# Kernel tuning notes

Measured on AMD Instinct MI355X. Metric: run time of the kernel, lower is better.

The kernel has to match this reference:

```python
import jax, jax.numpy as jnp
import numpy as np
from jax import lax

B, S, D, F = 2, 4096, 1024, 4096
LN_EPS = 1e-6

def _layer_norm(x, scale, bias):
    mu = jnp.mean(x, axis=-1, keepdims=True)
    var = jnp.mean(jnp.square(x - mu), axis=-1, keepdims=True)
    return (x - mu) * lax.rsqrt(var + LN_EPS) * scale + bias

def _gate_loop(q, k, v, a):
    # max-headed GateLoop: one head per channel, scalar complex state per channel
    # h_t = a_t * h_{t-1} + k_t * v_t ; y_t = q_t * h_t
    kv = (k * v).astype(jnp.complex64)
    def comb(e1, e2):
        a1, x1 = e1
        a2, x2 = e2
        return (a1 * a2, a2 * x1 + x2)
    _, h = lax.associative_scan(comb, (a, kv), axis=1)
    return q.astype(jnp.complex64) * h

def setup_inputs() -> dict:
    key = jax.random.key(0)
    ks = jax.random.split(key, 12)
    sd = 1.0 / np.sqrt(D)
    sf = 1.0 / np.sqrt(F)
    return {
        "x": jax.random.normal(ks[0], (B, S, D), jnp.float32),
        "Wq": jax.random.normal(ks[1], (D, D), jnp.float32) * sd,
        "Wk": jax.random.normal(ks[2], (D, D), jnp.float32) * sd,
        "Wv": jax.random.normal(ks[3], (D, D), jnp.float32) * sd,
        "Wa": jax.random.normal(ks[4], (D, 2 * D), jnp.float32) * sd,
        "Wg": jax.random.normal(ks[5], (D, D), jnp.float32) * sd,
        "Wo": jax.random.normal(ks[6], (D, D), jnp.float32) * sd,
        "ln1_scale": jnp.ones((D,), jnp.float32),
        "ln1_bias": jnp.zeros((D,), jnp.float32),
        "W1": jax.random.normal(ks[7], (D, F), jnp.float32) * sd,
        "b1": jax.random.normal(ks[8], (F,), jnp.float32) * 1e-6,
        "W2": jax.random.normal(ks[9], (F, D), jnp.float32) * sf,
        "b2": jax.random.normal(ks[10], (D,), jnp.float32) * 1e-6,
        "ln2_scale": jnp.ones((D,), jnp.float32),
        "ln2_bias": jnp.zeros((D,), jnp.float32),
    }

def reference(x, Wq, Wk, Wv, Wa, Wg, Wo, ln1_scale, ln1_bias, W1, b1, W2, b2, ln2_scale, ln2_bias):
    q = x @ Wq
    k = x @ Wk
    v = x @ Wv
    a = x @ Wa
    a_real, a_imag = jnp.split(a, 2, axis=-1)
    a_c = a_real + 1j * a_imag
    magnitude = jnp.abs(a_c)
    phase = jnp.angle(a_c)
    a_c = jax.nn.sigmoid(magnitude).astype(jnp.complex64) * jnp.exp(1j * phase)
    g = x.astype(jnp.complex64) @ Wg.astype(jnp.complex64)
    y = _gate_loop(q, k, v, a_c)
    y = y * (g * jax.nn.sigmoid(g))  # silu on complex g
    y = y @ Wo.astype(jnp.complex64)
    y = y.real
    # dropout deterministic (training=False)
    y = _layer_norm(y + x, ln1_scale, ln1_bias)
    h = jax.nn.gelu(y @ W1 + b1)
    out = h @ W2 + b2
    out = _layer_norm(out + y, ln2_scale, ln2_bias)
    return out
```

## Files before the change

### kernel.cpp

```cpp
#include <hip/hip_runtime.h>
#include <cstdint>

typedef unsigned short u16;
typedef unsigned int u32;

#define AS1 __attribute__((address_space(1)))
#define AS3 __attribute__((address_space(3)))

typedef _Float16 f16x8 __attribute__((ext_vector_type(8)));
typedef float f32x4 __attribute__((ext_vector_type(4)));

static constexpr int Bb = 2, Ss = 4096, Dd = 1024, Ff = 4096;
static constexpr int Mtok = Bb * Ss;
static constexpr int NCH = 128;
static constexpr int TCH = Ss / NCH;
static constexpr int PW = 6144;

__device__ __forceinline__ float h2f(u16 u) {
    union { u16 u; _Float16 h; } w; w.u = u; return (float)w.h;
}
__device__ __forceinline__ u16 f2h(float f) {
    union { _Float16 h; u16 u; } w; w.h = (_Float16)f; return w.u;
}

__device__ __forceinline__ float gelu_fast(float v) {
    float u = 1.5957691216057308f * (v + 0.044715f * v * v * v);
    return v / (1.f + __expf(-u));
}

__device__ __forceinline__ void gload_lds16(const u16* g, u16* l) {
    __builtin_amdgcn_global_load_lds((const AS1 u32*)g, (AS3 u32*)l, 16, 0, 0);
}

__global__ __launch_bounds__(256) void prep_fused(
    const float* __restrict__ x, u16* __restrict__ xb,
    const float* __restrict__ Wq, const float* __restrict__ Wk,
    const float* __restrict__ Wv, const float* __restrict__ Wa,
    const float* __restrict__ Wg, const float* __restrict__ Wo,
    const float* __restrict__ W1, const float* __restrict__ W2,
    u16* __restrict__ WTcat, u16* __restrict__ WTo,
    u16* __restrict__ WT1, u16* __restrict__ WT2) {
    __shared__ u16 t[32][33];
    const int tid = threadIdx.x;
    const int idx = blockIdx.x;
    if (idx < 8192) {
        const long i = ((long)idx * 256 + tid) * 4;
        float4 f = *(const float4*)(x + i);
        ushort4 o;
        o.x = f2h(f.x); o.y = f2h(f.y); o.z = f2h(f.z); o.w = f2h(f.w);
        *(ushort4*)(xb + i) = o;
        return;
    }
    const float* src; u16* dst; int K, N, ti;
    if (idx < 9216)       { src = Wq; dst = WTcat;             K = 1024; N = 1024; ti = idx - 8192; }
    else if (idx < 10240) { src = Wk; dst = WTcat + (1u << 20); K = 1024; N = 1024; ti = idx - 9216; }
    else if (idx < 11264) { src = Wv; dst = WTcat + (2u << 20); K = 1024; N = 1024; ti = idx - 10240; }
    else if (idx < 13312) { src = Wa; dst = WTcat + (3u << 20); K = 1024; N = 2048; ti = idx - 11264; }
    else if (idx < 14336) { src = Wg; dst = WTcat + (5u << 20); K = 1024; N = 1024; ti = idx - 13312; }
    else if (idx < 15360) { src = Wo; dst = WTo;               K = 1024; N = 1024; ti = idx - 14336; }
    else if (idx < 19456) { src = W1; dst = WT1;               K = 1024; N = 4096; ti = idx - 15360; }
    else                  { src = W2; dst = WT2;               K = 4096; N = 1024; ti = idx - 19456; }
    const int tiles_x = N >> 5;
    const int bx = ti % tiles_x, by = ti / tiles_x;
    const int n0 = bx << 5, k0 = by << 5;
    const int tx = tid & 31, ty = tid >> 5;
#pragma unroll
    for (int r = 0; r < 4; r++) {
        const int row = ty + r * 8;
        t[row][tx] = f2h(src[(long)(k0 + row) * N + n0 + tx]);
    }
    __syncthreads();
    const int cx = (tid & 15) << 1;
    const int ry = tid >> 4;
#pragma unroll
    for (int r = 0; r < 2; r++) {
        const int row = ry + r * 16;
        u32 v = (u32)t[cx][row] | ((u32)t[cx + 1][row] << 16);
        *(u32*)(dst + (long)(n0 + row) * K + k0 + cx) = v;
    }
}

template <int EPI>
__global__ __launch_bounds__(512, 2) void gemm8p(const u16* __restrict__ A,
                                                 const u16* __restrict__ BT,
                                                 u16* __restrict__ C,
                                                 const float* __restrict__ bias,
                                                 int M, int N, int K,
                                                 int lda, int ldc) {
    extern __shared__ u16 lds[];
    const int tid = threadIdx.x;

    const int ntn = N >> 8;
    const int total = (M >> 8) * ntn;
    const int tpb = total / (int)gridDim.x;
    const int cpx = total >> 3;

    const int srow = tid >> 3;
    const int scol = ((tid & 7) ^ (srow & 7)) << 3;
    const long lda64 = (long)lda << 6;
    const long ldb64 = (long)K << 6;

    const int nt = K >> 6;

    auto bases_for = [&](int t, int& tm, int& tn, const u16*& Ab, const u16*& Bb) {
        if (t > tpb - 1) t = tpb - 1;
        const int ti = (int)blockIdx.x + t * (int)gridDim.x;
        const int b = (ti & 7) * cpx + (ti >> 3);
        tm = (b / ntn) << 8;
        tn = (b % ntn) << 8;
        Ab = A + (long)(tm + srow) * lda + scol;
        Bb = BT + (long)(tn + srow) * (long)K + scol;
    };

    auto stA = [&](u16* bufbase, int h, const u16* Ab, int kt) {
        u16* d = bufbase + h * 8192 + tid * 8;
        const u16* g = Ab + (long)(h * 128) * lda + (kt << 6);
        gload_lds16(g, d);
        gload_lds16(g + lda64, d + 4096);
    };
    auto stB = [&](u16* bufbase, int h, const u16* Bb, int kt) {
        u16* d = bufbase + 16384 + h * 8192 + tid * 8;
        const u16* g = Bb + (long)(h * 128) * (long)K + (kt << 6);
        gload_lds16(g, d);
        gload_lds16(g + ldb64, d + 4096);
    };

    const int wid = tid >> 6, lane = tid & 63;
    const int r16 = lane & 15, q = lane >> 4;
    const int wm = (wid >> 2) * 128;
    const int wn = (wid & 3) * 64;
    const int r7 = r16 & 7;
    const int cx0 = (q ^ r7) << 3;
    const int cx1 = ((4 | q) ^ r7) << 3;
    const int aoff = (wm + r16) * 64;
    const int boff = 16384 + (wn + r16) * 64;

    f32x4 acc[8][4];
#pragma unroll
    for (int i = 0; i < 8; i++)
#pragma unroll
        for (int j = 0; j < 4; j++) acc[i][j] = (f32x4){0.f, 0.f, 0.f, 0.f};

    int tmc, tnc, tmn, tnn;
    const u16 *Ac, *Bc, *An, *Bn;
    bases_for(0, tmc, tnc, Ac, Bc);
    bases_for(1, tmn, tnn, An, Bn);

    stA(lds, 0, Ac, 0);
    stA(lds, 1, Ac, 0);
    stB(lds, 0, Bc, 0);
    stB(lds, 1, Bc, 0);
    stB(lds + 32768, 0, Bc, 1);
    stB(lds + 32768, 1, Bc, 1);

    for (int t = 0; t < tpb; ++t) {
        for (int it = 0; it < nt; ++it) {
            u16* sb = lds + ((it & 1) << 15);
            u16* so = lds + (((it & 1) ^ 1) << 15);

            asm volatile("s_waitcnt vmcnt(4)" ::: "memory");
            __builtin_amdgcn_s_barrier();

            f16x8 vb[4][2];
#pragma unroll
            for (int ni = 0; ni < 4; ni++) {
                vb[ni][0] = *(const f16x8*)(sb + boff + ni * 1024 + cx0);
                vb[ni][1] = *(const f16x8*)(sb + boff + ni * 1024 + cx1);
            }
            f16x8 pa[4][2];
#pragma unroll
            for (int m = 0; m < 4; m++) {
                pa[m][0] = *(const f16x8*)(sb + aoff + m * 1024 + cx0);
                pa[m][1] = *(const f16x8*)(sb + aoff + m * 1024 + cx1);
            }
            if (it + 1 < nt) {
                stA(so, 0, Ac, it + 1);
                stA(so, 1, Ac, it + 1);
            } else {
                stA(so, 0, An, 0);
                stA(so, 1, An, 0);
            }
            __builtin_amdgcn_s_barrier();
            asm volatile("s_waitcnt lgkmcnt(0)" ::: "memory");
            __builtin_amdgcn_s_setprio(1);
#pragma unroll
            for (int m = 0; m < 4; m++)
#pragma unroll
                for (int ni = 0; ni < 4; ni++) {
                    acc[m][ni] = __builtin_amdgcn_mfma_f32_16x16x32_f16(
                        pa[m][0], vb[ni][0], acc[m][ni], 0, 0, 0);
                    acc[m][ni] = __builtin_amdgcn_mfma_f32_16x16x32_f16(
                        pa[m][1], vb[ni][1], acc[m][ni], 0, 0, 0);
                }
            __builtin_amdgcn_s_setprio(0);
            __builtin_amdgcn_s_barrier();

#pragma unroll
            for (int m = 0; m < 4; m++) {
                pa[m][0] = *(const f16x8*)(sb + aoff + (4 + m) * 1024 + cx0);
                pa[m][1] = *(const f16x8*)(sb + aoff + (4 + m) * 1024 + cx1);
            }
            if (it + 2 < nt) {
                stB(sb, 0, Bc, it + 2);
                stB(sb, 1, Bc, it + 2);
            } else {
                stB(sb, 0, Bn, it + 2 - nt);
                stB(sb, 1, Bn, it + 2 - nt);
            }
            __builtin_amdgcn_s_barrier();
            asm volatile("s_waitcnt lgkmcnt(0)" ::: "memory");
            __builtin_amdgcn_s_setprio(1);
#pragma unroll
            for (int m = 0; m < 4; m++)
#pragma unroll
                for (int ni = 0; ni < 4; ni++) {
                    acc[4 + m][ni] = __builtin_amdgcn_mfma_f32_16x16x32_f16(
                        pa[m][0], vb[ni][0], acc[4 + m][ni], 0, 0, 0);
                    acc[4 + m][ni] = __builtin_amdgcn_mfma_f32_16x16x32_f16(
                        pa[m][1], vb[ni][1], acc[4 + m][ni], 0, 0, 0);
                }
            __builtin_amdgcn_s_setprio(0);
            __builtin_amdgcn_s_barrier();
        }

#pragma unroll
        for (int mi = 0; mi < 8; mi++) {
#pragma unroll
            for (int ni = 0; ni < 4; ni++) {
                const int gcol = tnc + wn + ni * 16 + r16;
                float bv = 0.f;
                if (EPI) bv = bias[gcol];
#pragma unroll
                for (int j = 0; j < 4; j++) {
                    const int grow = tmc + wm + mi * 16 + q * 4 + j;
                    float v = acc[mi][ni][j];
                    if (EPI) v += bv;
                    if (EPI == 1) v = gelu_fast(v);
                    C[(long)grow * ldc + gcol] = f2h(v);
                    acc[mi][ni][j] = 0.f;
                }
            }
        }
        tmc = tmn; tnc = tnn; Ac = An; Bc = Bn;
        bases_for(t + 2, tmn, tnn, An, Bn);
    }

    asm volatile("s_waitcnt vmcnt(0)" ::: "memory");
}

template <int EPI>
__global__ __launch_bounds__(512, 2) void gemm8p_n128(const u16* __restrict__ A,
                                                      const u16* __restrict__ BT,
                                                      u16* __restrict__ C,
                                                      const float* __restrict__ bias,
                                                      int M, int N, int K,
                                                      int lda, int ldc) {
    extern __shared__ u16 lds[];
    const int tid = threadIdx.x;

    const int ntn = N >> 7;
    int bid = blockIdx.x;
    {
        const int cpx = gridDim.x >> 3;
        bid = (bid & 7) * cpx + (bid >> 3);
    }
    const int tm = (bid / ntn) << 8;
    const int tn = (bid % ntn) << 7;

    const int srow = tid >> 3;
    const int scol = ((tid & 7) ^ (srow & 7)) << 3;
    const u16* Abase = A + (long)(tm + srow) * lda + scol;
    const u16* Bbase = BT + (long)(tn + srow) * (long)K + scol;
    const long lda64 = (long)lda << 6;
    const long ldb64 = (long)K << 6;

    const int nt = K >> 6;

    auto stA = [&](u16* bufbase, int h, int kt) {
        u16* d = bufbase + h * 8192 + tid * 8;
        const u16* g = Abase + (long)(h * 128) * lda + (kt << 6);
        gload_lds16(g, d);
        gload_lds16(g + lda64, d + 4096);
    };
    auto stB = [&](u16* bufbase, int kt) {
        u16* d = bufbase + 16384 + tid * 8;
        const u16* g = Bbase + (kt << 6);
        gload_lds16(g, d);
        gload_lds16(g + ldb64, d + 4096);
    };

    const int wid = tid >> 6, lane = tid & 63;
    const int r16 = lane & 15, q = lane >> 4;
    const int wm = (wid >> 1) * 64;
    const int wn = (wid & 1) * 64;
    const int r7 = r16 & 7;
    const int cx0 = (q ^ r7) << 3;
    const int cx1 = ((4 | q) ^ r7) << 3;
    const int aoff = (wm + r16) * 64;
    const int boff = 16384 + (wn + r16) * 64;

    f32x4 acc[4][4];
#pragma unroll
    for (int i = 0; i < 4; i++)
#pragma unroll
        for (int j = 0; j < 4; j++) acc[i][j] = (f32x4){0.f, 0.f, 0.f, 0.f};

    {
        const int t1 = nt > 1 ? 1 : 0;
        stA(lds, 0, 0);
        stA(lds, 1, 0);
        stB(lds, 0);
        stB(lds + 24576, t1);
    }

    for (int it = 0; it < nt; ++it) {
        u16* sb = lds + (it & 1) * 24576;
        u16* so = lds + ((it & 1) ^ 1) * 24576;
        const int tA = (it + 1 < nt) ? it + 1 : nt - 1;
        const int tB = (it + 2 < nt) ? it + 2 : nt - 1;

        asm volatile("s_waitcnt vmcnt(2)" ::: "memory");
        __builtin_amdgcn_s_barrier();

        f16x8 vb[4][2];
#pragma unroll
        for (int ni = 0; ni < 4; ni++) {
            vb[ni][0] = *(const f16x8*)(sb + boff + ni * 1024 + cx0);
            vb[ni][1] = *(const f16x8*)(sb + boff + ni * 1024 + cx1);
        }

#pragma unroll
        for (int p = 0; p < 2; ++p) {
            f16x8 pa[2][2];
#pragma unroll
            for (int m2 = 0; m2 < 2; m2++) {
                pa[m2][0] = *(const f16x8*)(sb + aoff + (2 * p + m2) * 1024 + cx0);
                pa[m2][1] = *(const f16x8*)(sb + aoff + (2 * p + m2) * 1024 + cx1);
            }
            if (p == 0) {
                stA(so, 0, tA);
            } else {
                stA(so, 1, tA);
                stB(sb, tB);
            }
            __builtin_amdgcn_s_barrier();
            asm volatile("s_waitcnt lgkmcnt(0)" ::: "memory");
            __builtin_amdgcn_s_setprio(1);
#pragma unroll
            for (int m2 = 0; m2 < 2; m2++)
#pragma unroll
                for (int ni = 0; ni < 4; ni++) {
                    acc[2 * p + m2][ni] = __builtin_amdgcn_mfma_f32_16x16x32_f16(
                        pa[m2][0], vb[ni][0], acc[2 * p + m2][ni], 0, 0, 0);
                    acc[2 * p + m2][ni] = __builtin_amdgcn_mfma_f32_16x16x32_f16(
                        pa[m2][1], vb[ni][1], acc[2 * p + m2][ni], 0, 0, 0);
                }
            __builtin_amdgcn_s_setprio(0);
            __builtin_amdgcn_s_barrier();
        }
    }

    asm volatile("s_waitcnt vmcnt(0)" ::: "memory");

#pragma unroll
    for (int mi = 0; mi < 4; mi++) {
#pragma unroll
        for (int ni = 0; ni < 4; ni++) {
            const int gcol = tn + wn + ni * 16 + r16;
            float bv = 0.f;
            if (EPI) bv = bias[gcol];
#pragma unroll
            for (int j = 0; j < 4; j++) {
                const int grow = tm + wm + mi * 16 + q * 4 + j;
                float v = acc[mi][ni][j];
                if (EPI) v += bv;
                if (EPI == 1) v = gelu_fast(v);
                C[(long)grow * ldc + gcol] = f2h(v);
            }
        }
    }
}

__device__ __forceinline__ void a_transform(float ar, float ai, float& cr, float& ci) {
    float m = sqrtf(ar * ar + ai * ai);
    float sg = 1.f / (1.f + __expf(-m));
    float sc = sg / fmaxf(m, 1e-30f);
    cr = ar * sc;
    ci = ai * sc;
}

__global__ __launch_bounds__(256) void scan1(const u16* __restrict__ pcat,
                                             float4* __restrict__ sum4) {
    const int b = blockIdx.y, c = blockIdx.x;
    const int d0 = threadIdx.x << 2;
    float Arp[4], Aip[4], Xr[4], Xi[4];
#pragma unroll
    for (int j = 0; j < 4; j++) { Arp[j] = 1.f; Aip[j] = 0.f; Xr[j] = 0.f; Xi[j] = 0.f; }
    const long rowbase = (long)b * Ss + (long)c * TCH;
#pragma unroll 2
    for (int s = 0; s < TCH; ++s) {
        const long ro = (rowbase + s) * PW;
        ushort4 uar = *(const ushort4*)(pcat + ro + 3072 + d0);
        ushort4 uai = *(const ushort4*)(pcat + ro + 4096 + d0);
        ushort4 ukk = *(const ushort4*)(pcat + ro + 1024 + d0);
        ushort4 uvv = *(const ushort4*)(pcat + ro + 2048 + d0);
        const u16* ear = (const u16*)&uar;
        const u16* eai = (const u16*)&uai;
        const u16* ekk = (const u16*)&ukk;
        const u16* evv = (const u16*)&uvv;
#pragma unroll
        for (int j = 0; j < 4; j++) {
            float cr, ci;
            a_transform(h2f(ear[j]), h2f(eai[j]), cr, ci);
            float kv = h2f(ekk[j]) * h2f(evv[j]);
            float nXr = cr * Xr[j] - ci * Xi[j] + kv;
            float nXi = cr * Xi[j] + ci * Xr[j];
            Xr[j] = nXr; Xi[j] = nXi;
            float nAr = cr * Arp[j] - ci * Aip[j];
            float nAi = cr * Aip[j] + ci * Arp[j];
            Arp[j] = nAr; Aip[j] = nAi;
        }
    }
    const long sbase = ((long)b * NCH + c) * 1024 + d0;
#pragma unroll
    for (int j = 0; j < 4; j++)
        sum4[sbase + j] = make_float4(Arp[j], Aip[j], Xr[j], Xi[j]);
}

__global__ __launch_bounds__(256) void scan2(const float4* __restrict__ sum4,
                                             float2* __restrict__ carry) {
    const int idx = blockIdx.x * 256 + threadIdx.x;
    const int b = idx >> 10, d = idx & 1023;
    float hr = 0.f, hi = 0.f;
    for (int cb = 0; cb < NCH / 8; ++cb) {
        float4 t[8];
#pragma unroll
        for (int j = 0; j < 8; j++)
            t[j] = sum4[((long)b * NCH + cb * 8 + j) * 1024 + d];
#pragma unroll
        for (int j = 0; j < 8; j++) {
            carry[((long)b * NCH + cb * 8 + j) * 1024 + d] = make_float2(hr, hi);
            float nr = t[j].x * hr - t[j].y * hi + t[j].z;
            float ni = t[j].x * hi + t[j].y * hr + t[j].w;
            hr = nr; hi = ni;
        }
    }
}

__global__ __launch_bounds__(256) void scan3(u16* pcat,
                                             const float2* __restrict__ carry) {
    const int b = blockIdx.y, c = blockIdx.x;
    const int d0 = threadIdx.x << 2;
    float hr[4], hi[4];
    const long cbase = ((long)b * NCH + c) * 1024 + d0;
#pragma unroll
    for (int j = 0; j < 4; j++) {
        float2 h0 = carry[cbase + j];
        hr[j] = h0.x; hi[j] = h0.y;
    }
    const long rowbase = (long)b * Ss + (long)c * TCH;
#pragma unroll 2
    for (int s = 0; s < TCH; ++s) {
        const long ro = (rowbase + s) * PW;
        ushort4 uar = *(const ushort4*)(pcat + ro + 3072 + d0);
        ushort4 uai = *(const ushort4*)(pcat + ro + 4096 + d0);
        ushort4 ukk = *(const ushort4*)(pcat + ro + 1024 + d0);
        ushort4 uvv = *(const ushort4*)(pcat + ro + 2048 + d0);
        ushort4 ugg = *(const ushort4*)(pcat + ro + 5120 + d0);
        ushort4 uqq = *(const ushort4*)(pcat + ro + d0);
        const u16* ear = (const u16*)&uar;
        const u16* eai = (const u16*)&uai;
        const u16* ekk = (const u16*)&ukk;
        const u16* evv = (const u16*)&uvv;
        const u16* egg = (const u16*)&ugg;
        const u16* eqq = (const u16*)&uqq;
        ushort4 oy;
        u16* ey = (u16*)&oy;
#pragma unroll
        for (int j = 0; j < 4; j++) {
            float cr, ci;
            a_transform(h2f(ear[j]), h2f(eai[j]), cr, ci);
            float kv = h2f(ekk[j]) * h2f(evv[j]);
            float nhr = cr * hr[j] - ci * hi[j] + kv;
            float nhi = cr * hi[j] + ci * hr[j];
            hr[j] = nhr; hi[j] = nhi;
            float gg = h2f(egg[j]);
            float si = gg / (1.f + __expf(-gg));
            ey[j] = f2h(h2f(eqq[j]) * nhr * si);
        }
        *(ushort4*)(pcat + ro + d0) = oy;
    }
}

template <int RESF32, int OUTF32>
__global__ __launch_bounds__(256) void ln_kernel(const u16* __restrict__ a, int sa,
                                                 const void* __restrict__ bres, int sres,
                                                 const float* __restrict__ scale,
                                                 const float* __restrict__ bias,
                                                 void* __restrict__ out, int sout) {
    const int row = blockIdx.x;
    const int tid = threadIdx.x;
    const long abase = (long)row * sa;
    const long rbase = (long)row * sres;
    const long obase = (long)row * sout;
    const int d0 = tid * 4;
    float v[4];
    ushort4 ua = *(const ushort4*)(a + abase + d0);
    const u16* ea = (const u16*)&ua;
    if (RESF32) {
        float4 rf = *(const float4*)((const float*)bres + rbase + d0);
        v[0] = h2f(ea[0]) + rf.x; v[1] = h2f(ea[1]) + rf.y;
        v[2] = h2f(ea[2]) + rf.z; v[3] = h2f(ea[3]) + rf.w;
    } else {
        ushort4 ur = *(const ushort4*)((const u16*)bres + rbase + d0);
        const u16* er = (const u16*)&ur;
#pragma unroll
        for (int j = 0; j < 4; j++) v[j] = h2f(ea[j]) + h2f(er[j]);
    }
    float s = v[0] + v[1] + v[2] + v[3];
    float s2 = v[0] * v[0] + v[1] * v[1] + v[2] * v[2] + v[3] * v[3];
#pragma unroll
    for (int off = 32; off; off >>= 1) {
        s += __shfl_down(s, off);
        s2 += __shfl_down(s2, off);
    }
    __shared__ float red[8];
    const int w = tid >> 6, lane = tid & 63;
    if (lane == 0) { red[w] = s; red[4 + w] = s2; }
    __syncthreads();
    if (tid == 0) {
        float ts = red[0] + red[1] + red[2] + red[3];
        float ts2 = red[4] + red[5] + red[6] + red[7];
        float mu = ts * (1.f / 1024.f);
        float var = ts2 * (1.f / 1024.f) - mu * mu;
        red[0] = mu;
        red[1] = rsqrtf(var + 1e-6f);
    }
    __syncthreads();
    const float mu = red[0], rs = red[1];
    float4 sc = *(const float4*)(scale + d0);
    float4 bi = *(const float4*)(bias + d0);
    float y0 = (v[0] - mu) * rs * sc.x + bi.x;
    float y1 = (v[1] - mu) * rs * sc.y + bi.y;
    float y2 = (v[2] - mu) * rs * sc.z + bi.z;
    float y3 = (v[3] - mu) * rs * sc.w + bi.w;
    if (OUTF32) {
        *(float4*)((float*)out + obase + d0) = make_float4(y0, y1, y2, y3);
    } else {
        ushort4 o;
        o.x = f2h(y0); o.y = f2h(y1); o.z = f2h(y2); o.w = f2h(y3);
        *(ushort4*)((u16*)out + obase + d0) = o;
    }
}

extern "C" void kernel_launch(void* const* d_in, const int* in_sizes, int n_in,
                              void* d_out, int out_size, void* d_ws, size_t ws_size,
                              hipStream_t stream) {
    const float* x    = (const float*)d_in[0];
    const float* Wq   = (const float*)d_in[1];
    const float* Wk   = (const float*)d_in[2];
    const float* Wv   = (const float*)d_in[3];
    const float* Wa   = (const float*)d_in[4];
    const float* Wg   = (const float*)d_in[5];
    const float* Wo   = (const float*)d_in[6];
    const float* ln1s = (const float*)d_in[7];
    const float* ln1b = (const float*)d_in[8];
    const float* W1   = (const float*)d_in[9];
    const float* b1   = (const float*)d_in[10];
    const float* W2   = (const float*)d_in[11];
    const float* b2   = (const float*)d_in[12];
    const float* ln2s = (const float*)d_in[13];
    const float* ln2b = (const float*)d_in[14];

    u16* ws    = (u16*)d_ws;
    u16* xb    = ws;
    u16* WTcat = xb + (8u << 20);
    u16* WTo   = WTcat + (6u << 20);
    u16* WT1   = WTo + (1u << 20);
    u16* WT2   = WT1 + (4u << 20);
    u16* pcat  = WT2 + (4u << 20);

    float4* sum4  = (float4*)WTcat;
    float2* carry = (float2*)(WTcat + (2u << 20));

    static bool attr_done = false;
    if (!attr_done) {
        hipFuncSetAttribute(reinterpret_cast<const void*>(&gemm8p<0>),
                            hipFuncAttributeMaxDynamicSharedMemorySize, 131072);
        hipFuncSetAttribute(reinterpret_cast<const void*>(&gemm8p<1>),
                            hipFuncAttributeMaxDynamicSharedMemorySize, 131072);
        hipFuncSetAttribute(reinterpret_cast<const void*>(&gemm8p_n128<0>),
                            hipFuncAttributeMaxDynamicSharedMemorySize, 98304);
        hipFuncSetAttribute(reinterpret_cast<const void*>(&gemm8p_n128<2>),
                            hipFuncAttributeMaxDynamicSharedMemorySize, 98304);
        attr_done = true;
    }


    prep_fused<<<dim3(23552), dim3(256), 0, stream>>>(x, xb, Wq, Wk, Wv, Wa, Wg, Wo,
                                                      W1, W2, WTcat, WTo, WT1, WT2);

    gemm8p<0><<<dim3(256), dim3(512), 131072, stream>>>(xb, WTcat, pcat, nullptr,
                                                        Mtok, PW, 1024, 1024, PW);
    scan1<<<dim3(NCH, Bb), dim3(256), 0, stream>>>(pcat, sum4);
    scan2<<<dim3(8), dim3(256), 0, stream>>>(sum4, carry);
    scan3<<<dim3(NCH, Bb), dim3(256), 0, stream>>>(pcat, carry);
    gemm8p_n128<0><<<dim3(256), dim3(512), 98304, stream>>>(pcat, WTo, pcat + 1024,
                                                            nullptr,
                                                            Mtok, 1024, 1024, PW, PW);
    ln_kernel<1, 0><<<dim3(Mtok), dim3(256), 0, stream>>>(pcat + 1024, PW, x, 1024,
                                                          ln1s, ln1b, pcat, PW);
    gemm8p<1><<<dim3(256), dim3(512), 131072, stream>>>(pcat, WT1, pcat + 2048, b1,
                                                        Mtok, Ff, 1024, PW, PW);
    gemm8p_n128<2><<<dim3(256), dim3(512), 98304, stream>>>(pcat + 2048, WT2,
                                                            pcat + 1024, b2,
                                                            Mtok, 1024, Ff, PW, PW);
    ln_kernel<0, 1><<<dim3(Mtok), dim3(256), 0, stream>>>(pcat + 1024, PW, pcat, PW,
                                                          ln2s, ln2b, d_out, 1024);
}
```

Measured before the change: 513.4 us.

## Restructure GEMM main loops to split K-halves and cut barriers

Both GEMM inner loops now split each K-tile into two halves (cx0 and cx1). The first half's fragments are loaded up front, and the second half's A fragments are reloaded one at a time, interleaved with the MFMAs under sched_barrier. This removes two of the four s_barriers per iteration and lowers register pressure by holding one fragment set instead of two. The intent is less synchronisation stall and better overlap of LDS reads with MFMA work. In exchange, the LDS-buffer reuse and vmcnt waits must be reasoned about carefully to avoid races, and the waits at tile boundaries were changed to match.

```diff
diff --git a/kernel.cpp b/kernel.cpp
--- a/kernel.cpp
+++ b/kernel.cpp
@@ -158,21 +158,18 @@
             u16* sb = lds + ((it & 1) << 15);
             u16* so = lds + (((it & 1) ^ 1) << 15);
 
-            asm volatile("s_waitcnt vmcnt(4)" ::: "memory");
+            if (it != 0 || t == 0)
+                asm volatile("s_waitcnt vmcnt(4)" ::: "memory");
             __builtin_amdgcn_s_barrier();
 
-            f16x8 vb[4][2];
-#pragma unroll
-            for (int ni = 0; ni < 4; ni++) {
-                vb[ni][0] = *(const f16x8*)(sb + boff + ni * 1024 + cx0);
-                vb[ni][1] = *(const f16x8*)(sb + boff + ni * 1024 + cx1);
-            }
-            f16x8 pa[4][2];
-#pragma unroll
-            for (int m = 0; m < 4; m++) {
-                pa[m][0] = *(const f16x8*)(sb + aoff + m * 1024 + cx0);
-                pa[m][1] = *(const f16x8*)(sb + aoff + m * 1024 + cx1);
-            }
+            f16x8 vb[4], pa[8];
+#pragma unroll
+            for (int ni = 0; ni < 4; ni++)
+                vb[ni] = *(const f16x8*)(sb + boff + ni * 1024 + cx0);
+#pragma unroll
+            for (int m = 0; m < 8; m++)
+                pa[m] = *(const f16x8*)(sb + aoff + m * 1024 + cx0);
+            __builtin_amdgcn_sched_barrier(0);
             if (it + 1 < nt) {
                 stA(so, 0, Ac, it + 1);
                 stA(so, 1, Ac, it + 1);
@@ -180,26 +177,28 @@
                 stA(so, 0, An, 0);
                 stA(so, 1, An, 0);
             }
+            asm volatile("s_waitcnt lgkmcnt(0)" ::: "memory");
+            __builtin_amdgcn_sched_barrier(0);
+
+            __builtin_amdgcn_s_setprio(1);
+#pragma unroll
+            for (int m = 0; m < 8; m++) {
+#pragma unroll
+                for (int ni = 0; ni < 4; ni++)
+                    acc[m][ni] = __builtin_amdgcn_mfma_f32_16x16x32_f16(
+                        pa[m], vb[ni], acc[m][ni], 0, 0, 0);
+                __builtin_amdgcn_sched_barrier(0);
+                pa[m] = *(const f16x8*)(sb + aoff + m * 1024 + cx1);
+                __builtin_amdgcn_sched_barrier(0);
+            }
+            __builtin_amdgcn_s_setprio(0);
+#pragma unroll
+            for (int ni = 0; ni < 4; ni++)
+                vb[ni] = *(const f16x8*)(sb + boff + ni * 1024 + cx1);
+            asm volatile("s_waitcnt lgkmcnt(0)" ::: "memory");
+            __builtin_amdgcn_sched_barrier(0);
             __builtin_amdgcn_s_barrier();
-            asm volatile("s_waitcnt lgkmcnt(0)" ::: "memory");
-            __builtin_amdgcn_s_setprio(1);
-#pragma unroll
-            for (int m = 0; m < 4; m++)
-#pragma unroll
-                for (int ni = 0; ni < 4; ni++) {
-                    acc[m][ni] = __builtin_amdgcn_mfma_f32_16x16x32_f16(
-                        pa[m][0], vb[ni][0], acc[m][ni], 0, 0, 0);
-                    acc[m][ni] = __builtin_amdgcn_mfma_f32_16x16x32_f16(
-                        pa[m][1], vb[ni][1], acc[m][ni], 0, 0, 0);
-                }
-            __builtin_amdgcn_s_setprio(0);
-            __builtin_amdgcn_s_barrier();
-
-#pragma unroll
-            for (int m = 0; m < 4; m++) {
-                pa[m][0] = *(const f16x8*)(sb + aoff + (4 + m) * 1024 + cx0);
-                pa[m][1] = *(const f16x8*)(sb + aoff + (4 + m) * 1024 + cx1);
-            }
+
             if (it + 2 < nt) {
                 stB(sb, 0, Bc, it + 2);
                 stB(sb, 1, Bc, it + 2);
@@ -207,21 +206,18 @@
                 stB(sb, 0, Bn, it + 2 - nt);
                 stB(sb, 1, Bn, it + 2 - nt);
             }
-            __builtin_amdgcn_s_barrier();
-            asm volatile("s_waitcnt lgkmcnt(0)" ::: "memory");
+
             __builtin_amdgcn_s_setprio(1);
 #pragma unroll
-            for (int m = 0; m < 4; m++)
-#pragma unroll
-                for (int ni = 0; ni < 4; ni++) {
-                    acc[4 + m][ni] = __builtin_amdgcn_mfma_f32_16x16x32_f16(
-                        pa[m][0], vb[ni][0], acc[4 + m][ni], 0, 0, 0);
-                    acc[4 + m][ni] = __builtin_amdgcn_mfma_f32_16x16x32_f16(
-                        pa[m][1], vb[ni][1], acc[4 + m][ni], 0, 0, 0);
-                }
+            for (int m = 0; m < 8; m++)
+#pragma unroll
+                for (int ni = 0; ni < 4; ni++)
+                    acc[m][ni] = __builtin_amdgcn_mfma_f32_16x16x32_f16(
+                        pa[m], vb[ni], acc[m][ni], 0, 0, 0);
             __builtin_amdgcn_s_setprio(0);
-            __builtin_amdgcn_s_barrier();
         }
+
+        asm volatile("s_waitcnt vmcnt(4)" ::: "memory");
 
 #pragma unroll
         for (int mi = 0; mi < 8; mi++) {
@@ -322,42 +318,48 @@
         asm volatile("s_waitcnt vmcnt(2)" ::: "memory");
         __builtin_amdgcn_s_barrier();
 
-        f16x8 vb[4][2];
-#pragma unroll
-        for (int ni = 0; ni < 4; ni++) {
-            vb[ni][0] = *(const f16x8*)(sb + boff + ni * 1024 + cx0);
-            vb[ni][1] = *(const f16x8*)(sb + boff + ni * 1024 + cx1);
+        f16x8 vb[4], pa[4];
+#pragma unroll
+        for (int ni = 0; ni < 4; ni++)
+            vb[ni] = *(const f16x8*)(sb + boff + ni * 1024 + cx0);
+#pragma unroll
+        for (int m = 0; m < 4; m++)
+            pa[m] = *(const f16x8*)(sb + aoff + m * 1024 + cx0);
+        __builtin_amdgcn_sched_barrier(0);
+        stA(so, 0, tA);
+        stA(so, 1, tA);
+        asm volatile("s_waitcnt lgkmcnt(0)" ::: "memory");
+        __builtin_amdgcn_sched_barrier(0);
+
+        __builtin_amdgcn_s_setprio(1);
+#pragma unroll
+        for (int m = 0; m < 4; m++) {
+#pragma unroll
+            for (int ni = 0; ni < 4; ni++)
+                acc[m][ni] = __builtin_amdgcn_mfma_f32_16x16x32_f16(
+                    pa[m], vb[ni], acc[m][ni], 0, 0, 0);
+            __builtin_amdgcn_sched_barrier(0);
+            pa[m] = *(const f16x8*)(sb + aoff + m * 1024 + cx1);
+            __builtin_amdgcn_sched_barrier(0);
         }
-
-#pragma unroll
-        for (int p = 0; p < 2; ++p) {
-            f16x8 pa[2][2];
-#pragma unroll
-            for (int m2 = 0; m2 < 2; m2++) {
-                pa[m2][0] = *(const f16x8*)(sb + aoff + (2 * p + m2) * 1024 + cx0);
-                pa[m2][1] = *(const f16x8*)(sb + aoff + (2 * p + m2) * 1024 + cx1);
-            }
-            if (p == 0) {
-                stA(so, 0, tA);
-            } else {
-                stA(so, 1, tA);
-                stB(sb, tB);
-            }
-            __builtin_amdgcn_s_barrier();
-            asm volatile("s_waitcnt lgkmcnt(0)" ::: "memory");
-            __builtin_amdgcn_s_setprio(1);
-#pragma unroll
-            for (int m2 = 0; m2 < 2; m2++)
-#pragma unroll
-                for (int ni = 0; ni < 4; ni++) {
-                    acc[2 * p + m2][ni] = __builtin_amdgcn_mfma_f32_16x16x32_f16(
-                        pa[m2][0], vb[ni][0], acc[2 * p + m2][ni], 0, 0, 0);
-                    acc[2 * p + m2][ni] = __builtin_amdgcn_mfma_f32_16x16x32_f16(
-                        pa[m2][1], vb[ni][1], acc[2 * p + m2][ni], 0, 0, 0);
-                }
-            __builtin_amdgcn_s_setprio(0);
-            __builtin_amdgcn_s_barrier();
-        }
+        __builtin_amdgcn_s_setprio(0);
+#pragma unroll
+        for (int ni = 0; ni < 4; ni++)
+            vb[ni] = *(const f16x8*)(sb + boff + ni * 1024 + cx1);
+        asm volatile("s_waitcnt lgkmcnt(0)" ::: "memory");
+        __builtin_amdgcn_sched_barrier(0);
+        __builtin_amdgcn_s_barrier();
+
+        stB(sb, tB);
+
+        __builtin_amdgcn_s_setprio(1);
+#pragma unroll
+        for (int m = 0; m < 4; m++)
+#pragma unroll
+            for (int ni = 0; ni < 4; ni++)
+                acc[m][ni] = __builtin_amdgcn_mfma_f32_16x16x32_f16(
+                    pa[m], vb[ni], acc[m][ni], 0, 0, 0);
+        __builtin_amdgcn_s_setprio(0);
     }
 
     asm volatile("s_waitcnt vmcnt(0)" ::: "memory");
```

Result: slower. 531.2 us (+3.5%).
